# Kernel optimization log

Measured on AMD Instinct MI355X. Metric: run time of the kernel, lower is better.

## Reference

```python
import jax, jax.numpy as jnp
import numpy as np

GRID_SIZE, K, NUM_EXPERTS = 5, 3, 8
N_MLP, N_KAN = 4, 4
B, D, H, O = 4096, 512, 2048, 512


def _bspline_basis(x, grid, k):
    """Cox-de Boor recursion, vectorized. x: [B, D]; grid: [G]. Returns [B, D, G-k-1]."""
    xe = x[..., None]
    # order-0: indicator of grid interval
    b = ((grid[:-1] <= xe) & (xe < grid[1:])).astype(x.dtype)  # [B, D, G-1]
    for kk in range(1, k + 1):
        t_i = grid[: -(kk + 1)]
        t_ik = grid[kk:-1]
        t_ik1 = grid[kk + 1:]
        t_i1 = grid[1:-kk]
        left = (xe - t_i) / (t_ik - t_i) * b[..., :-1]
        right = (t_ik1 - xe) / (t_ik1 - t_i1) * b[..., 1:]
        b = left + right
    return b


def setup_inputs() -> dict:
    key = jax.random.key(0)
    ks = jax.random.split(key, 8)
    x = jax.random.normal(ks[0], (B, D), dtype=jnp.float32)
    # Router output: binary expert mask; rows with no active group fall back to expert 7
    mask = (jax.random.uniform(ks[1], (B, NUM_EXPERTS)) < 0.3).astype(jnp.float32)
    other = jnp.zeros((NUM_EXPERTS,), jnp.float32).at[7].set(1.0)
    expert_mask = jnp.where(mask.sum(axis=1, keepdims=True) == 0, other[None, :], mask)
    s_d = 1.0 / np.sqrt(D)
    s_h = 1.0 / np.sqrt(H)
    gate_w = jax.random.normal(ks[2], (D, NUM_EXPERTS), jnp.float32) * s_d
    gate_b = jnp.zeros((NUM_EXPERTS,), jnp.float32)
    mlp_w1 = jax.random.normal(ks[3], (N_MLP, D, H), jnp.float32) * s_d
    mlp_b1 = jnp.zeros((N_MLP, H), jnp.float32)
    mlp_w2 = jax.random.normal(ks[4], (N_MLP, H, O), jnp.float32) * s_h
    mlp_b2 = jnp.zeros((N_MLP, O), jnp.float32)
    kan_scaling = jnp.ones((N_KAN, D, O), jnp.float32)
    kan_coeff = jax.random.normal(ks[5], (N_KAN, D, O, GRID_SIZE + K), jnp.float32)
    return dict(x=x, expert_mask=expert_mask, gate_w=gate_w, gate_b=gate_b,
                mlp_w1=mlp_w1, mlp_b1=mlp_b1, mlp_w2=mlp_w2, mlp_b2=mlp_b2,
                kan_scaling=kan_scaling, kan_coeff=kan_coeff)


def reference(x, expert_mask, gate_w, gate_b, mlp_w1, mlp_b1, mlp_w2, mlp_b2,
              kan_scaling, kan_coeff):
    # gate softmax + router mask + renormalize
    gate = jax.nn.softmax(x @ gate_w + gate_b, axis=1)          # [B, E]
    masked = gate * expert_mask
    w = masked / (masked.sum(axis=1, keepdims=True) + 1e-9)      # [B, E]

    # MLP experts (eval mode -> dropout is identity)
    h = jax.nn.relu(jnp.einsum('bd,edh->ebh', x, mlp_w1) + mlp_b1[:, None, :])
    mlp_out = jnp.einsum('ebh,eho->ebo', h, mlp_w2) + mlp_b2[:, None, :]  # [4, B, O]

    # KAN experts: uniform grid extended by k knots each side (spacing 2/grid_size)
    hg = 2.0 / GRID_SIZE
    grid = jnp.arange(GRID_SIZE + 2 * K + 1, dtype=x.dtype) * hg - (1.0 + K * hg)
    basis = _bspline_basis(x, grid, K)                           # [B, D, 8]
    ceff = kan_coeff * kan_scaling[..., None]                    # [4, D, O, 8]
    kan_out = jnp.einsum('big,eiog->ebo', basis, ceff)           # [4, B, O]

    expert_outputs = jnp.concatenate([mlp_out, kan_out], axis=0)  # [8, B, O]
    out = jnp.einsum('ebo,be->bo', expert_outputs, w)             # [B, O]
    return out, expert_mask, w
```

## Files before the change

### kernel.cpp

```cpp
#include <hip/hip_runtime.h>

typedef __attribute__((ext_vector_type(4))) float f32x4;
typedef __attribute__((ext_vector_type(8))) __bf16 bf16x8;
typedef __attribute__((ext_vector_type(4))) unsigned short u16x4;
typedef __attribute__((ext_vector_type(8))) unsigned short u16x8;

#define NB 4096
#define ND 512
#define NH 2048
#define NO 512

__device__ __forceinline__ unsigned short f2bf(float f) {
  unsigned int u = __float_as_uint(f);
  u += 0x7fffu + ((u >> 16) & 1u);
  return (unsigned short)(u >> 16);
}
__device__ __forceinline__ float bf2f(unsigned short u) {
  return __uint_as_float(((unsigned int)u) << 16);
}
__device__ __forceinline__ void gload_lds16(const void* g, void* l) {
  __builtin_amdgcn_global_load_lds(
      (const __attribute__((address_space(1))) unsigned int*)g,
      (__attribute__((address_space(3))) unsigned int*)l, 16, 0, 0);
}
__device__ __forceinline__ size_t paddr(int row, int k, int Mtot) {
  int kt = k >> 5, c = (k >> 3) & 3, el = k & 7;
  return ((size_t)kt * Mtot + row) * 32 + (size_t)((c ^ ((row >> 1) & 3)) * 8 + el);
}

__global__ void gate_kernel(const float* __restrict__ x, const float* __restrict__ emask,
                            const float* __restrict__ gw, const float* __restrict__ gb,
                            float* __restrict__ w_out, float* __restrict__ mask_out) {
  int b = blockIdx.x;
  int lane = threadIdx.x;
  float l8[8] = {0,0,0,0,0,0,0,0};
  const float* xr = x + (size_t)b * ND;
  for (int d = lane; d < ND; d += 64) {
    float xv = xr[d];
    const float* g = gw + d * 8;
#pragma unroll
    for (int e = 0; e < 8; ++e) l8[e] = fmaf(xv, g[e], l8[e]);
  }
#pragma unroll
  for (int off = 32; off > 0; off >>= 1) {
#pragma unroll
    for (int e = 0; e < 8; ++e) l8[e] += __shfl_xor(l8[e], off);
  }
  float m = -1e30f;
#pragma unroll
  for (int e = 0; e < 8; ++e) { l8[e] += gb[e]; m = fmaxf(m, l8[e]); }
  float s = 0.f, p[8];
#pragma unroll
  for (int e = 0; e < 8; ++e) { p[e] = expf(l8[e] - m); s += p[e]; }
  float inv = 1.f / s;
  float mk[8], me[8], ms = 0.f;
#pragma unroll
  for (int e = 0; e < 8; ++e) {
    mk[e] = emask[(size_t)b * 8 + e];
    me[e] = p[e] * inv * mk[e];
    ms += me[e];
  }
  float winv = 1.f / (ms + 1e-9f);
  if (lane == 0) {
#pragma unroll
    for (int e = 0; e < 8; ++e) {
      w_out[(size_t)b * 8 + e] = me[e] * winv;
      mask_out[(size_t)b * 8 + e] = mk[e];
    }
  }
}

__global__ void cast_x_kernel(const float* __restrict__ x, unsigned short* __restrict__ xb) {
  size_t t = (size_t)blockIdx.x * 256 + threadIdx.x;
  int b = (int)(t >> 6);
  int k0 = ((int)t & 63) * 8;
  const f32x4* px = (const f32x4*)(x + (size_t)b * ND + k0);
  f32x4 v0 = px[0], v1 = px[1];
  u16x8 r;
#pragma unroll
  for (int j = 0; j < 4; ++j) { r[j] = f2bf(v0[j]); r[4 + j] = f2bf(v1[j]); }
  *(u16x8*)(xb + paddr(b, k0, NB)) = r;
}

__global__ void basis_kernel(const float* __restrict__ x, unsigned short* __restrict__ bas) {
  size_t t = (size_t)blockIdx.x * 256 + threadIdx.x;
  int b = (int)(t >> 9);
  int i = (int)(t & 511);
  float xv = x[t];
  const float hg = 0.4f;
  float tt[12];
#pragma unroll
  for (int j = 0; j < 12; ++j) tt[j] = -2.2f + hg * (float)j;
  float b0[11];
#pragma unroll
  for (int j = 0; j < 11; ++j) b0[j] = (tt[j] <= xv && xv < tt[j + 1]) ? 1.f : 0.f;
  float b1[10], b2[9], b3[8];
#pragma unroll
  for (int j = 0; j < 10; ++j) b1[j] = ((xv - tt[j]) * b0[j] + (tt[j + 2] - xv) * b0[j + 1]) * (1.f / (1.f * hg));
#pragma unroll
  for (int j = 0; j < 9; ++j)  b2[j] = ((xv - tt[j]) * b1[j] + (tt[j + 3] - xv) * b1[j + 1]) * (1.f / (2.f * hg));
#pragma unroll
  for (int j = 0; j < 8; ++j)  b3[j] = ((xv - tt[j]) * b2[j] + (tt[j + 4] - xv) * b2[j + 1]) * (1.f / (3.f * hg));
  u16x8 r;
#pragma unroll
  for (int j = 0; j < 8; ++j) r[j] = f2bf(b3[j]);
  *(u16x8*)(bas + paddr(b, i * 8, NB)) = r;
}

__global__ void transpose_cast(const float* __restrict__ in, unsigned short* __restrict__ outp,
                               int R, int Cc) {
  __shared__ float tile[32][33];
  int e = blockIdx.z;
  int c0 = blockIdx.x * 32, r0 = blockIdx.y * 32;
  int tx = threadIdx.x & 31, ty = threadIdx.x >> 5;
  const float* ine = in + (size_t)e * R * Cc;
  unsigned short* oute = outp + (size_t)e * R * Cc;
#pragma unroll
  for (int j = 0; j < 32; j += 8)
    tile[ty + j][tx] = ine[(size_t)(r0 + ty + j) * Cc + (c0 + tx)];
  __syncthreads();
#pragma unroll
  for (int j = 0; j < 32; j += 8)
    oute[paddr(c0 + ty + j, r0 + tx, Cc)] = f2bf(tile[tx][ty + j]);
}

__global__ void make_cefft(const float* __restrict__ coeff, const float* __restrict__ scal,
                           unsigned short* __restrict__ outp) {
  size_t t = (size_t)blockIdx.x * 256 + threadIdx.x;
  int i = (int)(t & 511);
  int o = (int)((t >> 9) & 511);
  int e = (int)(t >> 18);
  size_t io = ((size_t)e * 512 + i) * 512 + o;
  const f32x4* cp = (const f32x4*)(coeff + io * 8);
  f32x4 c0 = cp[0], c1 = cp[1];
  float s = scal[io];
  u16x8 r;
#pragma unroll
  for (int j = 0; j < 4; ++j) r[j] = f2bf(c0[j] * s);
#pragma unroll
  for (int j = 0; j < 4; ++j) r[4 + j] = f2bf(c1[j] * s);
  *(u16x8*)(outp + (size_t)e * NO * (ND * 8) + paddr(o, i * 8, NO)) = r;
}

struct GemmArgs {
  const unsigned short* A; size_t sAe; int Ma;
  const unsigned short* B; size_t sBe; int Mb;
  const float* bias; int sBias;
  unsigned short* C; size_t sCe; size_t sHalf; int ldc;
  int Kspan; int zshift; int gx; int nxy;
  int mode;
};

__global__ __launch_bounds__(512, 2) void gemm_fused(int nL1, GemmArgs a1, GemmArgs a2) {
  __shared__ __align__(16) char lsA[3 * 16384];
  __shared__ __align__(16) char lsB[3 * 16384];
  const int wg = blockIdx.x;
  const GemmArgs g = (wg < nL1) ? a1 : a2;
  const int wgl = (wg < nL1) ? wg : wg - nL1;
  const int tid = threadIdx.x;
  const int lane = tid & 63, wid = tid >> 6;
  const int wr = wid >> 2, wc = wid & 3;
  const int z = wgl / g.nxy;
  int rem = wgl % g.nxy;
  rem = (rem & 7) * (g.nxy >> 3) + (rem >> 3);
  const int bcol = (rem % g.gx) * 256;
  const int brow = (rem / g.gx) * 256;
  const int e = z >> g.zshift;
  const int half = z & ((1 << g.zshift) - 1);
  const int ktBase = half * (g.Kspan >> 5);
  const unsigned short* Ae = g.A + (size_t)e * g.sAe;
  const unsigned short* Be = g.B + (size_t)e * g.sBe;
  const int Ma = g.Ma, Mb = g.Mb;
  const int NT = g.Kspan >> 5;

  const int fr = lane & 15, fc = lane >> 4;
  const int sR = tid >> 2, ssc = tid & 3;

  auto stage = [&](int buf, int t2) {
#pragma unroll
    for (int q = 0; q < 2; ++q) {
      const unsigned short* src =
          Ae + ((size_t)(ktBase + t2) * Ma + (brow + q * 128 + sR)) * 32 + ssc * 8;
      gload_lds16(src, lsA + buf * 16384 + q * 8192 + tid * 16);
    }
#pragma unroll
    for (int q = 0; q < 2; ++q) {
      const unsigned short* src =
          Be + ((size_t)(ktBase + t2) * Mb + (bcol + q * 128 + sR)) * 32 + ssc * 8;
      gload_lds16(src, lsB + buf * 16384 + q * 8192 + tid * 16);
    }
  };

  f32x4 acc[8][4] = {};

  stage(0, 0);
  stage(1, 1);
  asm volatile("s_waitcnt vmcnt(4)" ::: "memory");
  __builtin_amdgcn_s_barrier();

  int bi = 0;
  for (int t = 0; t < NT; ++t) {
    const char* bA = lsA + bi * 16384;
    const char* bB = lsB + bi * 16384;
    const int pb = (bi == 0) ? 2 : bi - 1;
    const bool pf = (t + 2 < NT);

    bf16x8 af[8], bfrag[4];
#pragma unroll
    for (int i = 0; i < 8; ++i) {
      int ra = wr * 128 + i * 16 + fr;
      af[i] = *(const bf16x8*)(bA + ra * 64 + ((fc ^ ((ra >> 1) & 3)) << 4));
    }
#pragma unroll
    for (int n = 0; n < 4; ++n) {
      int rb = wc * 64 + n * 16 + fr;
      bfrag[n] = *(const bf16x8*)(bB + rb * 64 + ((fc ^ ((rb >> 1) & 3)) << 4));
    }
    if (pf) stage(pb, t + 2);
#pragma unroll
    for (int mi = 0; mi < 8; ++mi)
#pragma unroll
      for (int ni = 0; ni < 4; ++ni)
        acc[mi][ni] = __builtin_amdgcn_mfma_f32_16x16x32_bf16(bfrag[ni], af[mi], acc[mi][ni], 0, 0, 0);
    if (pf)               asm volatile("s_waitcnt vmcnt(4)" ::: "memory");
    else if (t + 1 < NT)  asm volatile("s_waitcnt vmcnt(0)" ::: "memory");
    __builtin_amdgcn_s_barrier();

    bi = (bi == 2) ? 0 : bi + 1;
  }

  unsigned short* Ce = g.C + (size_t)e * g.sCe + (size_t)half * g.sHalf;
  const int ldc = g.ldc;
#pragma unroll
  for (int mi = 0; mi < 8; ++mi) {
    int row = brow + wr * 128 + mi * 16 + fr;
#pragma unroll
    for (int ni = 0; ni < 4; ++ni) {
      int col0 = bcol + wc * 64 + ni * 16 + (fc << 2);
      u16x4 r;
      if (g.mode == 0) {
        f32x4 bv = *(const f32x4*)(g.bias + e * g.sBias + col0);
#pragma unroll
        for (int j = 0; j < 4; ++j) r[j] = f2bf(fmaxf(acc[mi][ni][j] + bv[j], 0.f));
        *(u16x4*)(Ce + paddr(row, col0, NB)) = r;
      } else {
#pragma unroll
        for (int j = 0; j < 4; ++j) r[j] = f2bf(acc[mi][ni][j]);
        *(u16x4*)(Ce + (size_t)row * ldc + col0) = r;
      }
    }
  }
}

__global__ void combine_kernel(const unsigned short* __restrict__ eoM,
                               const unsigned short* __restrict__ eoK,
                               const float* __restrict__ b2,
                               const float* __restrict__ w, float* __restrict__ out) {
  int b = blockIdx.x;
  int o = threadIdx.x * 4;
  float wv[8];
#pragma unroll
  for (int e = 0; e < 8; ++e) wv[e] = w[(size_t)b * 8 + e];
  f32x4 acc = {0.f, 0.f, 0.f, 0.f};
#pragma unroll
  for (int e = 0; e < 4; ++e) {
    u16x4 m0 = *(const u16x4*)(eoM + ((size_t)e * NB + b) * NO + o);
    u16x4 m1 = *(const u16x4*)(eoM + ((size_t)(4 + e) * NB + b) * NO + o);
    f32x4 bb = *(const f32x4*)(b2 + e * NO + o);
#pragma unroll
    for (int j = 0; j < 4; ++j)
      acc[j] = fmaf(wv[e], bf2f(m0[j]) + bf2f(m1[j]) + bb[j], acc[j]);
  }
#pragma unroll
  for (int e = 0; e < 4; ++e) {
    u16x4 k0 = *(const u16x4*)(eoK + ((size_t)e * NB + b) * NO + o);
    u16x4 k1 = *(const u16x4*)(eoK + ((size_t)(4 + e) * NB + b) * NO + o);
#pragma unroll
    for (int j = 0; j < 4; ++j)
      acc[j] = fmaf(wv[4 + e], bf2f(k0[j]) + bf2f(k1[j]), acc[j]);
  }
  *(f32x4*)(out + (size_t)b * NO + o) = acc;
}

extern "C" void kernel_launch(void* const* d_in, const int* in_sizes, int n_in,
                              void* d_out, int out_size, void* d_ws, size_t ws_size,
                              hipStream_t stream) {
  (void)in_sizes; (void)n_in; (void)out_size;
  const float* x      = (const float*)d_in[0];
  const float* emask  = (const float*)d_in[1];
  const float* gate_w = (const float*)d_in[2];
  const float* gate_b = (const float*)d_in[3];
  const float* mlp_w1 = (const float*)d_in[4];
  const float* mlp_b1 = (const float*)d_in[5];
  const float* mlp_w2 = (const float*)d_in[6];
  const float* mlp_b2 = (const float*)d_in[7];
  const float* kan_s  = (const float*)d_in[8];
  const float* kan_c  = (const float*)d_in[9];

  float* out = (float*)d_out;
  float* mask_out = out + (size_t)NB * NO;
  float* w_out    = mask_out + (size_t)NB * 8;

  char* ws = (char*)d_ws;
  size_t off = 0;
  auto take = [&](size_t bytes) { size_t r = off; off += (bytes + 255) & ~(size_t)255; return r; };
  unsigned short* w1t   = (unsigned short*)(ws + take((size_t)4 * NH * ND * 2));
  unsigned short* w2t   = (unsigned short*)(ws + take((size_t)4 * NO * NH * 2));
  unsigned short* cefft = (unsigned short*)(ws + take((size_t)4 * NO * (ND * 8) * 2));
  unsigned short* xbf   = (unsigned short*)(ws + take((size_t)NB * ND * 2));
  unsigned short* regA  = (unsigned short*)(ws + take((size_t)8 * NB * NO * 2));
  unsigned short* hbuf  = (unsigned short*)(ws + take((size_t)4 * NB * NH * 2));
  size_t base_need = off;
  size_t eoK_off = base_need;
  const bool fused = (ws_size >= base_need + (size_t)8 * NB * NO * 2);
  unsigned short* eoM = regA;
  unsigned short* bas, *eoK;
  if (fused) {
    bas = regA;
    eoK = (unsigned short*)(ws + eoK_off);
  } else {
    bas = hbuf;
    eoK = (unsigned short*)((char*)hbuf + (size_t)2 * NB * NH * 2);
  }

  gate_kernel<<<NB, 64, 0, stream>>>(x, emask, gate_w, gate_b, w_out, mask_out);
  cast_x_kernel<<<(NB * ND / 8) / 256, 256, 0, stream>>>(x, xbf);
  transpose_cast<<<dim3(NH / 32, ND / 32, 4), 256, 0, stream>>>(mlp_w1, w1t, ND, NH);
  transpose_cast<<<dim3(NO / 32, NH / 32, 4), 256, 0, stream>>>(mlp_w2, w2t, NH, NO);
  make_cefft<<<(4 * ND * NO) / 256, 256, 0, stream>>>(kan_c, kan_s, cefft);

  GemmArgs aL1 = { xbf, 0, NB,
                   w1t, (size_t)NH * ND, NH,
                   mlp_b1, NH,
                   hbuf, (size_t)NB * NH, 0, NH,
                   ND, 0, NH / 256, (NH / 256) * (NB / 256), 0 };
  GemmArgs aL2 = { hbuf, (size_t)NB * NH, NB,
                   w2t, (size_t)NO * NH, NO,
                   nullptr, 0,
                   eoM, (size_t)NB * NO, (size_t)4 * NB * NO, NO,
                   NH / 2, 1, NO / 256, (NO / 256) * (NB / 256), 2 };
  GemmArgs aL3 = { bas, 0, NB,
                   cefft, (size_t)NO * (ND * 8), NO,
                   nullptr, 0,
                   eoK, (size_t)NB * NO, (size_t)4 * NB * NO, NO,
                   (ND * 8) / 2, 1, NO / 256, (NO / 256) * (NB / 256), 2 };

  if (fused) {
    basis_kernel<<<(NB * ND) / 256, 256, 0, stream>>>(x, bas);
    gemm_fused<<<512 + 256, 512, 0, stream>>>(512, aL1, aL3);
    gemm_fused<<<256, 512, 0, stream>>>(0, aL2, aL2);
  } else {
    gemm_fused<<<512, 512, 0, stream>>>(512, aL1, aL1);
    gemm_fused<<<256, 512, 0, stream>>>(0, aL2, aL2);
    basis_kernel<<<(NB * ND) / 256, 256, 0, stream>>>(x, bas);
    gemm_fused<<<256, 512, 0, stream>>>(0, aL3, aL3);
  }

  combine_kernel<<<NB, NO / 4, 0, stream>>>(eoM, eoK, mlp_b2, w_out, out);
}
```

Baseline: 219.8 us.

## Restructure GEMM main loop into 8-phase ping-pong schedule with 128KB LDS

```diff
diff --git a/kernel.cpp b/kernel.cpp
--- a/kernel.cpp
+++ b/kernel.cpp
@@ -152,8 +152,7 @@
 };
 
 __global__ __launch_bounds__(512, 2) void gemm_fused(int nL1, GemmArgs a1, GemmArgs a2) {
-  __shared__ __align__(16) char lsA[3 * 16384];
-  __shared__ __align__(16) char lsB[3 * 16384];
+  __shared__ __align__(16) char ls[131072];
   const int wg = blockIdx.x;
   const GemmArgs g = (wg < nL1) ? a1 : a2;
   const int wgl = (wg < nL1) ? wg : wg - nL1;
@@ -171,85 +170,99 @@
   const unsigned short* Ae = g.A + (size_t)e * g.sAe;
   const unsigned short* Be = g.B + (size_t)e * g.sBe;
   const int Ma = g.Ma, Mb = g.Mb;
-  const int NT = g.Kspan >> 5;
+  const int NT = g.Kspan >> 6;
+  const int NI = NT >> 1;
 
   const int fr = lane & 15, fc = lane >> 4;
-  const int sR = tid >> 2, ssc = tid & 3;
-
-  auto stage = [&](int buf, int t2) {
-#pragma unroll
-    for (int q = 0; q < 2; ++q) {
-      const unsigned short* src =
-          Ae + ((size_t)(ktBase + t2) * Ma + (brow + q * 128 + sR)) * 32 + ssc * 8;
-      gload_lds16(src, lsA + buf * 16384 + q * 8192 + tid * 16);
-    }
-#pragma unroll
-    for (int q = 0; q < 2; ++q) {
-      const unsigned short* src =
-          Be + ((size_t)(ktBase + t2) * Mb + (bcol + q * 128 + sR)) * 32 + ssc * 8;
-      gload_lds16(src, lsB + buf * 16384 + q * 8192 + tid * 16);
-    }
+
+  auto stA = [&](int S, int T, int ks) {
+    const char* src = (const char*)Ae + ((size_t)(ktBase + 2 * T + ks) * Ma + brow) * 64;
+    char* dst = ls + S * 32768 + ks * 16384;
+    gload_lds16(src + tid * 16, dst + tid * 16);
+    gload_lds16(src + 8192 + tid * 16, dst + 8192 + tid * 16);
   };
+  auto stB = [&](int S, int T, int ks) {
+    const char* src = (const char*)Be + ((size_t)(ktBase + 2 * T + ks) * Mb + bcol) * 64;
+    char* dst = ls + 65536 + S * 32768 + ks * 16384;
+    gload_lds16(src + tid * 16, dst + tid * 16);
+    gload_lds16(src + 8192 + tid * 16, dst + 8192 + tid * 16);
+  };
 
   f32x4 acc[8][4] = {};
-
-  stage(0, 0);
-  stage(1, 1);
+  bf16x8 af[4], bfrag[4];
+
+#define PH(S, KS, M, NEWB, STG, WT)                                              \
+  do {                                                                           \
+    if (NEWB) {                                                                  \
+      _Pragma("unroll") for (int ni = 0; ni < 4; ++ni) {                         \
+        int r = wc * 64 + ni * 16 + fr;                                          \
+        bfrag[ni] = *(const bf16x8*)(ls + 65536 + (S) * 32768 + (KS) * 16384 +   \
+                                     r * 64 + ((fc ^ ((r >> 1) & 3)) << 4));     \
+      }                                                                          \
+    }                                                                            \
+    _Pragma("unroll") for (int mi = 0; mi < 4; ++mi) {                           \
+      int r = (M) * 128 + mi * 32 + wr * 16 + fr;                                \
+      af[mi] = *(const bf16x8*)(ls + (S) * 32768 + (KS) * 16384 +                \
+                                r * 64 + ((fc ^ ((r >> 1) & 3)) << 4));          \
+    }                                                                            \
+    STG;                                                                         \
+    __builtin_amdgcn_s_barrier();                                                \
+    asm volatile("s_waitcnt lgkmcnt(0)" ::: "memory");                           \
+    __builtin_amdgcn_sched_barrier(0);                                           \
+    __builtin_amdgcn_s_setprio(1);                                               \
+    _Pragma("unroll") for (int mi = 0; mi < 4; ++mi)                             \
+      _Pragma("unroll") for (int ni = 0; ni < 4; ++ni)                           \
+        acc[(M) * 4 + mi][ni] = __builtin_amdgcn_mfma_f32_16x16x32_bf16(         \
+            bfrag[ni], af[mi], acc[(M) * 4 + mi][ni], 0, 0, 0);                  \
+    __builtin_amdgcn_s_setprio(0);                                               \
+    WT;                                                                          \
+    __builtin_amdgcn_s_barrier();                                                \
+  } while (0)
+
+  stA(0, 0, 0); stB(0, 0, 0); stA(0, 0, 1); stB(0, 0, 1); stA(1, 1, 0); stB(1, 1, 0);
   asm volatile("s_waitcnt vmcnt(4)" ::: "memory");
   __builtin_amdgcn_s_barrier();
 
-  int bi = 0;
-  for (int t = 0; t < NT; ++t) {
-    const char* bA = lsA + bi * 16384;
-    const char* bB = lsB + bi * 16384;
-    const int pb = (bi == 0) ? 2 : bi - 1;
-    const bool pf = (t + 2 < NT);
-
-    bf16x8 af[8], bfrag[4];
-#pragma unroll
-    for (int i = 0; i < 8; ++i) {
-      int ra = wr * 128 + i * 16 + fr;
-      af[i] = *(const bf16x8*)(bA + ra * 64 + ((fc ^ ((ra >> 1) & 3)) << 4));
-    }
-#pragma unroll
-    for (int n = 0; n < 4; ++n) {
-      int rb = wc * 64 + n * 16 + fr;
-      bfrag[n] = *(const bf16x8*)(bB + rb * 64 + ((fc ^ ((rb >> 1) & 3)) << 4));
-    }
-    if (pf) stage(pb, t + 2);
-#pragma unroll
-    for (int mi = 0; mi < 8; ++mi)
-#pragma unroll
-      for (int ni = 0; ni < 4; ++ni)
-        acc[mi][ni] = __builtin_amdgcn_mfma_f32_16x16x32_bf16(bfrag[ni], af[mi], acc[mi][ni], 0, 0, 0);
-    if (pf)               asm volatile("s_waitcnt vmcnt(4)" ::: "memory");
-    else if (t + 1 < NT)  asm volatile("s_waitcnt vmcnt(0)" ::: "memory");
-    __builtin_amdgcn_s_barrier();
-
-    bi = (bi == 2) ? 0 : bi + 1;
-  }
+  for (int i = 0; i < NI; ++i) {
+    const int T0 = 2 * i, T1 = 2 * i + 1;
+    const bool pf = (i + 1 < NI);
+    PH(0, 0, 0, true,  { stA(1, T1, 1); }, {});
+    PH(0, 0, 1, false, { stB(1, T1, 1); },
+       { asm volatile("s_waitcnt vmcnt(4)" ::: "memory"); });
+    PH(0, 1, 0, true,  { if (pf) stA(0, T0 + 2, 0); }, {});
+    PH(0, 1, 1, false, { if (pf) stB(0, T0 + 2, 0); }, {});
+    PH(1, 0, 0, true,  { if (pf) stA(0, T0 + 2, 1); }, {});
+    PH(1, 0, 1, false, { if (pf) stB(0, T0 + 2, 1); },
+       { if (pf) asm volatile("s_waitcnt vmcnt(4)" ::: "memory");
+         else    asm volatile("s_waitcnt vmcnt(0)" ::: "memory"); });
+    PH(1, 1, 0, true,  { if (pf) stA(1, T1 + 2, 0); }, {});
+    PH(1, 1, 1, false, { if (pf) stB(1, T1 + 2, 0); }, {});
+  }
+#undef PH
 
   unsigned short* Ce = g.C + (size_t)e * g.sCe + (size_t)half * g.sHalf;
   const int ldc = g.ldc;
 #pragma unroll
-  for (int mi = 0; mi < 8; ++mi) {
-    int row = brow + wr * 128 + mi * 16 + fr;
-#pragma unroll
-    for (int ni = 0; ni < 4; ++ni) {
-      int col0 = bcol + wc * 64 + ni * 16 + (fc << 2);
-      u16x4 r;
-      if (g.mode == 0) {
-        f32x4 bv = *(const f32x4*)(g.bias + e * g.sBias + col0);
-#pragma unroll
-        for (int j = 0; j < 4; ++j) r[j] = f2bf(fmaxf(acc[mi][ni][j] + bv[j], 0.f));
-        *(u16x4*)(Ce + paddr(row, col0, NB)) = r;
-      } else {
-#pragma unroll
-        for (int j = 0; j < 4; ++j) r[j] = f2bf(acc[mi][ni][j]);
-        *(u16x4*)(Ce + (size_t)row * ldc + col0) = r;
+  for (int m = 0; m < 2; ++m)
+#pragma unroll
+    for (int mi = 0; mi < 4; ++mi) {
+      int row = brow + m * 128 + mi * 32 + wr * 16 + fr;
+#pragma unroll
+      for (int ni = 0; ni < 4; ++ni) {
+        int col0 = bcol + wc * 64 + ni * 16 + (fc << 2);
+        u16x4 r;
+        if (g.mode == 0) {
+          f32x4 bv = *(const f32x4*)(g.bias + e * g.sBias + col0);
+#pragma unroll
+          for (int j = 0; j < 4; ++j) r[j] = f2bf(fmaxf(acc[m * 4 + mi][ni][j] + bv[j], 0.f));
+          *(u16x4*)(Ce + paddr(row, col0, NB)) = r;
+        } else {
+#pragma unroll
+          for (int j = 0; j < 4; ++j) r[j] = f2bf(acc[m * 4 + mi][ni][j]);
+          *(u16x4*)(Ce + (size_t)row * ldc + col0) = r;
+        }
       }
     }
-  }
 }
 
 __global__ void combine_kernel(const unsigned short* __restrict__ eoM,
```

After: 220.6 us. About the same (+0.4%).
